# Optimization experiments

Hardware: AMD Instinct MI355X
Metric: run time of the kernel (lower is better)

Reference implementation:

```python
import jax, jax.numpy as jnp
import numpy as np

NUM_TOKENS = 4096
IN_FEATURES = 4096
OUT_FEATURES = 4096
MAX_PACKED = 4


def setup_inputs() -> dict:
    key = jax.random.key(0)
    k1, k2, k3 = jax.random.split(key, 3)
    x = jax.random.normal(k1, (NUM_TOKENS, IN_FEATURES), dtype=jnp.float32)
    weight_stacked = jax.random.normal(
        k2, (MAX_PACKED, OUT_FEATURES, IN_FEATURES), dtype=jnp.float32) * 0.02
    indices = jax.random.randint(k3, (NUM_TOKENS,), 0, MAX_PACKED, dtype=jnp.int32)
    return {"x": x, "weight_stacked": weight_stacked, "indices": indices}


def reference(x, weight_stacked, indices):
    # apply_swap: outputs[t] = x[t] @ weight_stacked[indices[t]].T
    # Grouped-GEMM expressed as E dense GEMMs with masked combine
    # (E = max_packed is a small static constant).
    E = weight_stacked.shape[0]
    out = jnp.zeros((x.shape[0], weight_stacked.shape[1]), dtype=x.dtype)
    for e in range(E):
        sel = (indices == e)[:, None].astype(x.dtype)  # [T,1]
        out = out + sel * jnp.einsum('ti,oi->to', x, weight_stacked[e])
    return out
```

## Files before the change

### kernel.cpp

```cpp
#include <hip/hip_runtime.h>

#define T 4096
#define K 4096
#define O 4096
#define E 4
#define BK 64
#define MAXT128 35

typedef __attribute__((ext_vector_type(8))) short bf16x8;
typedef __attribute__((ext_vector_type(4))) float f32x4;

__device__ __forceinline__ unsigned short f2bf(float f) {
  unsigned int u = __float_as_uint(f);
  u += 0x7fffu + ((u >> 16) & 1u);
  return (unsigned short)(u >> 16);
}

__global__ void build_meta(const int* __restrict__ idx, int* __restrict__ perm,
                           int* __restrict__ meta, int4* __restrict__ t256,
                           int4* __restrict__ t128, int4* __restrict__ sched) {
  const int wave = threadIdx.x >> 6;
  const int lane = threadIdx.x & 63;
  __shared__ int s_off[E + 1];
  __shared__ int rtE[20], rtP[20], rtC[20];
  __shared__ int r_sh;
  int total = 0;
  for (int t0 = 0; t0 < T; t0 += 64)
    total += __popcll(__ballot(idx[t0 + lane] == wave));
  if (lane == 0) s_off[wave + 1] = total;
  __syncthreads();
  if (threadIdx.x == 0) {
    s_off[0] = 0;
    for (int e = 0; e < E; e++) s_off[e + 1] += s_off[e];
  }
  __syncthreads();
  int base = s_off[wave];
  const unsigned long long below = (1ull << lane) - 1ull;
  for (int t0 = 0; t0 < T; t0 += 64) {
    int e = idx[t0 + lane];
    unsigned long long m = __ballot(e == wave);
    if (e == wave) perm[base + __popcll(m & below)] = t0 + lane;
    base += __popcll(m);
  }
  if (threadIdx.x == 0) {
    int n = 0;
    for (int e = 0; e < E; e++) {
      int s = s_off[e], c = s_off[e + 1] - s;
      for (int ro = 0; ro < c; ro += 256) {
        rtE[n] = e; rtP[n] = s + ro; rtC[n] = (c - ro) < 256 ? (c - ro) : 256; n++;
      }
    }
    r_sh = n;
    meta[0] = n * 16;
    int n1 = 0;
    for (int e = 0; e < E; e++) {
      int s = s_off[e], c = s_off[e + 1] - s;
      for (int ro = 0; ro < c; ro += 128)
        t128[n1++] = make_int4(e, s + ro, (c - ro) < 128 ? (c - ro) : 128, 0);
    }
    for (; n1 < MAXT128; n1++) t128[n1] = make_int4(-1, 0, 0, 0);
  }
  __syncthreads();
  const int r = r_sh;
  for (int i = threadIdx.x; i < 16 * r; i += 256)
    t256[i] = make_int4(rtE[i >> 4], rtP[i >> 4], rtC[i >> 4], (i & 15) * 256);
  {
    const int b = threadIdx.x;
    const int ru = r - 16;
    const int xcd = b & 7, s = b >> 3;
    const int rt_ = 4 * (xcd >> 1) + (s >> 3);
    const int nt_ = 8 * (xcd & 1) + (s & 7);
    sched[b * 3 + 0] = make_int4(rt_ * 16 + nt_, 0, 16, 0);
    int sgi = 1, u0 = b * ru, u1 = u0 + ru;
    while (u0 < u1) {
      int tI = 256 + (u0 >> 4), q0 = u0 & 15;
      int avail = 16 - q0, want = u1 - u0;
      int take = want < avail ? want : avail;
      sched[b * 3 + sgi] = make_int4(tI, q0, take, 0);
      sgi++; u0 += take;
    }
    for (; sgi < 3; sgi++) sched[b * 3 + sgi] = make_int4(-1, 0, 0, 0);
  }
}

__global__ void zero_rem(const int* __restrict__ meta, const int4* __restrict__ t256,
                         const int* __restrict__ perm, float* __restrict__ out) {
  const int ntiles = meta[0];
  const int tI = 256 + (int)blockIdx.x / 16;
  if (tI >= ntiles) return;
  const int4 td = t256[tI];
  const int rt = (blockIdx.x & 15) * 16 + ((int)threadIdx.x >> 4);
  if (rt >= td.z) return;
  float4* p = (float4*)(out + (size_t)perm[td.y + rt] * O + td.w) + (threadIdx.x & 15) * 4;
  const float4 z = {0.f, 0.f, 0.f, 0.f};
  p[0] = z; p[1] = z; p[2] = z; p[3] = z;
}

__global__ void convert_kernel(const float4* __restrict__ w4, const float* __restrict__ x,
                               const int* __restrict__ perm,
                               ushort4* __restrict__ wb4, ushort4* __restrict__ xg4) {
  const size_t NW4 = (size_t)E * O * K / 4;
  const size_t NX4 = (size_t)T * K / 4;
  const size_t stride = (size_t)gridDim.x * blockDim.x;
  const size_t t0 = (size_t)blockIdx.x * blockDim.x + threadIdx.x;
  for (size_t i = t0; i < NW4; i += stride) {
    float4 v = w4[i];
    wb4[i] = make_ushort4(f2bf(v.x), f2bf(v.y), f2bf(v.z), f2bf(v.w));
  }
  for (size_t j = t0; j < NX4; j += stride) {
    int p = (int)(j >> 10);
    int c = (int)(j & 1023);
    float4 v = *((const float4*)(x + (size_t)perm[p] * K) + c);
    xg4[j] = make_ushort4(f2bf(v.x), f2bf(v.y), f2bf(v.z), f2bf(v.w));
  }
}

__global__ __launch_bounds__(512, 2)
void gemm8p(const unsigned short* __restrict__ xg, const unsigned short* __restrict__ wbb,
            const int* __restrict__ perm, const int4* __restrict__ t256,
            const int4* __restrict__ sched, float* __restrict__ out) {
  __shared__ unsigned short lds[65536];
  const int bid = blockIdx.x;
  const int tid = threadIdx.x;
  const int wid = tid >> 6, lane = tid & 63;
  const int wr = wid >> 2, wc = wid & 3;
  const int kc4 = lane >> 4;
  unsigned short* ldsw = &lds[wid * 512];

#define GLL(gp, lp) __builtin_amdgcn_global_load_lds( \
    (const __attribute__((address_space(1))) void*)(gp), \
    (__attribute__((address_space(3))) void*)(lp), 16, 0, 0)
#define STAGE_A(bo, kh, ko) do { \
    GLL(srcA0 + (ko) + (kh) * 32, ldsw + (bo) + (kh) * 8192); \
    GLL(srcA1 + (ko) + (kh) * 32, ldsw + (bo) + (kh) * 8192 + 4096); \
  } while (0)
#define STAGE_B(bo, kh, ko) do { \
    GLL(srcB0 + (ko) + (kh) * 32, ldsw + (bo) + 16384 + (kh) * 8192); \
    GLL(srcB1 + (ko) + (kh) * 32, ldsw + (bo) + 16384 + (kh) * 8192 + 4096); \
  } while (0)
#define LOADA(dst, bo, ks, mh) do { _Pragma("unroll") \
    for (int mi = 0; mi < 4; ++mi) \
      dst[mi] = *(const bf16x8*)&lds[(bo) + (ks) * 8192 + aoff[mh][mi]]; } while (0)
#define LOADB(dst, bo, ks) do { _Pragma("unroll") \
    for (int ni = 0; ni < 4; ++ni) \
      dst[ni] = *(const bf16x8*)&lds[(bo) + 16384 + (ks) * 8192 + boff[ni]]; } while (0)
#define MFMA16(A, B, mh) do { _Pragma("unroll") \
    for (int mi = 0; mi < 4; ++mi) _Pragma("unroll") \
      for (int ni = 0; ni < 4; ++ni) \
        acc[(mh) * 4 + mi][ni] = __builtin_amdgcn_mfma_f32_16x16x32_bf16( \
            A[mi], B[ni], acc[(mh) * 4 + mi][ni], 0, 0, 0); } while (0)
#define BAR() do { __builtin_amdgcn_s_barrier(); asm volatile("" ::: "memory"); } while (0)
#define VM4() asm volatile("s_waitcnt vmcnt(4)" ::: "memory")
#define VM0() asm volatile("s_waitcnt vmcnt(0)" ::: "memory")
#define PRIO1() __builtin_amdgcn_s_setprio(1)
#define PRIO0() __builtin_amdgcn_s_setprio(0)

#define KTILE(C, X, koe) do { \
    const int ko = (koe); \
    LOADA(afP, C, 0, 0); LOADB(bfP, C, 0); \
    STAGE_A(X, 0, ko); \
    PRIO1(); MFMA16(afP, bfP, 0); PRIO0(); \
    LOADA(afQ, C, 0, 1); \
    STAGE_B(X, 0, ko); \
    PRIO1(); MFMA16(afQ, bfP, 1); PRIO0(); \
    VM4(); BAR(); \
    LOADA(afP, C, 1, 0); LOADB(bfQ, C, 1); \
    STAGE_A(X, 1, ko); \
    PRIO1(); MFMA16(afP, bfQ, 0); PRIO0(); \
    LOADA(afQ, C, 1, 1); \
    STAGE_B(X, 1, ko); \
    PRIO1(); MFMA16(afQ, bfQ, 1); PRIO0(); \
    VM4(); BAR(); \
  } while (0)

  int aoff[2][4], boff[4];
#pragma unroll
  for (int mh = 0; mh < 2; ++mh)
#pragma unroll
    for (int mi = 0; mi < 4; ++mi) {
      int r = wr * 128 + mh * 64 + mi * 16 + (lane & 15);
      aoff[mh][mi] = (((r >> 1) << 3) + (((((r & 1) << 2) | kc4)) ^ ((r >> 1) & 7))) * 8;
    }
#pragma unroll
  for (int ni = 0; ni < 4; ++ni) {
    int r = wc * 64 + ni * 16 + (lane & 15);
    boff[ni] = (((r >> 1) << 3) + (((((r & 1) << 2) | kc4)) ^ ((r >> 1) & 7))) * 8;
  }

  for (int sg = 0; sg < 3; ++sg) {
    const int4 sd = sched[bid * 3 + sg];
    if (sd.x < 0) break;
    const int4 td = t256[sd.x];
    const int e = td.x, p0 = td.y, rc = td.z, n0 = td.w;
    const int kt0 = sd.y << 2;
    const int nt = sd.z << 2;

    const unsigned short *srcA0, *srcA1, *srcB0, *srcB1;
    {
      const unsigned short* wB = wbb + (size_t)e * O * K + (size_t)n0 * K;
      int s0 = tid, s1 = 512 + tid;
      int b0 = s0 >> 3, v0 = (s0 & 7) ^ (b0 & 7);
      int r0 = b0 * 2 + (v0 >> 2), c0 = v0 & 3;
      int b1 = s1 >> 3, v1 = (s1 & 7) ^ (b1 & 7);
      int r1 = b1 * 2 + (v1 >> 2), c1 = v1 & 3;
      int ra0 = r0 < rc ? r0 : rc - 1;
      int ra1 = r1 < rc ? r1 : rc - 1;
      srcA0 = xg + (size_t)(p0 + ra0) * K + c0 * 8;
      srcA1 = xg + (size_t)(p0 + ra1) * K + c1 * 8;
      srcB0 = wB + (size_t)r0 * K + c0 * 8;
      srcB1 = wB + (size_t)r1 * K + c1 * 8;
    }

    f32x4 acc[8][4] = {};
    bf16x8 afP[4], afQ[4], bfP[4], bfQ[4];

    const int kb = kt0 << 6;
    STAGE_A(0, 0, kb); STAGE_B(0, 0, kb);
    STAGE_A(0, 1, kb); STAGE_B(0, 1, kb);
    VM4(); BAR();

    for (int tp = 0; tp < nt; tp += 2) {
      KTILE(0, 32768, ((tp + 1 < nt ? tp + 1 : tp) + kt0) << 6);
      KTILE(32768, 0, ((tp + 2 < nt ? tp + 2 : tp + 1) + kt0) << 6);
    }
    VM0();

    if (sd.z == 16) {
#pragma unroll
      for (int mh = 0; mh < 2; ++mh)
#pragma unroll
        for (int mi = 0; mi < 4; ++mi) {
          const int rbase = wr * 128 + mh * 64 + mi * 16 + (lane >> 4) * 4;
#pragma unroll
          for (int reg = 0; reg < 4; ++reg) {
            const int pr = rbase + reg;
            if (pr < rc) {
              float* orow = out + (size_t)perm[p0 + pr] * O + n0 + wc * 64 + (lane & 15);
#pragma unroll
              for (int ni = 0; ni < 4; ++ni) orow[ni * 16] = acc[mh * 4 + mi][ni][reg];
            }
          }
        }
    } else {
#pragma unroll
      for (int mh = 0; mh < 2; ++mh)
#pragma unroll
        for (int mi = 0; mi < 4; ++mi) {
          const int rbase = wr * 128 + mh * 64 + mi * 16 + (lane >> 4) * 4;
#pragma unroll
          for (int reg = 0; reg < 4; ++reg) {
            const int pr = rbase + reg;
            if (pr < rc) {
              float* orow = out + (size_t)perm[p0 + pr] * O + n0 + wc * 64 + (lane & 15);
#pragma unroll
              for (int ni = 0; ni < 4; ++ni)
                unsafeAtomicAdd(&orow[ni * 16], acc[mh * 4 + mi][ni][reg]);
            }
          }
        }
    }
  }
}

__global__ __launch_bounds__(256)
void gemm_fb(const float* __restrict__ xf, const float* __restrict__ wf,
             const int* __restrict__ perm, const int4* __restrict__ tiles,
             float* __restrict__ out) {
  __shared__ unsigned short lds_a[128 * 64];
  __shared__ unsigned short lds_b[128 * 64];
  const int4 td = tiles[blockIdx.x];
  if (td.x < 0) return;
  const int e = td.x, p0 = td.y, rc = td.z;
  const int n0 = blockIdx.y * 128;
  const int wave = threadIdx.x >> 6, lane = threadIdx.x & 63;
  const int wr = wave >> 1, wc = wave & 1;
  f32x4 acc[4][4] = {};
  const float* wf_base = wf + (size_t)e * O * K + (size_t)n0 * K;
  for (int k0 = 0; k0 < K; k0 += 64) {
    if (k0) __syncthreads();
#pragma unroll
    for (int i = 0; i < 8; i++) {
      int l4 = i * 256 + (int)threadIdx.x;
      int row = l4 >> 4;
      int c4 = (l4 & 15) << 2;
      int ra = row < rc ? row : (rc - 1);
      const float4 va = *(const float4*)(xf + (size_t)perm[p0 + ra] * K + k0 + c4);
      *(ushort4*)&lds_a[row * 64 + c4] = make_ushort4(f2bf(va.x), f2bf(va.y), f2bf(va.z), f2bf(va.w));
      const float4 vb = *(const float4*)(wf_base + (size_t)row * K + k0 + c4);
      *(ushort4*)&lds_b[row * 64 + c4] = make_ushort4(f2bf(vb.x), f2bf(vb.y), f2bf(vb.z), f2bf(vb.w));
    }
    __syncthreads();
#pragma unroll
    for (int ks = 0; ks < 2; ks++) {
      bf16x8 a2[4], b2[4];
#pragma unroll
      for (int mi = 0; mi < 4; mi++)
        a2[mi] = *(const bf16x8*)&lds_a[(wr * 64 + mi * 16 + (lane & 15)) * 64 + ks * 32 + (lane >> 4) * 8];
#pragma unroll
      for (int ni = 0; ni < 4; ni++)
        b2[ni] = *(const bf16x8*)&lds_b[(wc * 64 + ni * 16 + (lane & 15)) * 64 + ks * 32 + (lane >> 4) * 8];
#pragma unroll
      for (int mi = 0; mi < 4; mi++)
#pragma unroll
        for (int ni = 0; ni < 4; ni++)
          acc[mi][ni] = __builtin_amdgcn_mfma_f32_16x16x32_bf16(a2[mi], b2[ni], acc[mi][ni], 0, 0, 0);
    }
  }
#pragma unroll
  for (int mi = 0; mi < 4; mi++) {
    const int rb = wr * 64 + mi * 16 + (lane >> 4) * 4;
#pragma unroll
    for (int reg = 0; reg < 4; reg++) {
      const int rt = rb + reg;
      if (rt < rc) {
        float* orow = out + (size_t)perm[p0 + rt] * O + n0 + wc * 64 + (lane & 15);
#pragma unroll
        for (int ni = 0; ni < 4; ni++) orow[ni * 16] = acc[mi][ni][reg];
      }
    }
  }
}

extern "C" void kernel_launch(void* const* d_in, const int* in_sizes, int n_in,
                              void* d_out, int out_size, void* d_ws, size_t ws_size,
                              hipStream_t stream) {
  const float* x = (const float*)d_in[0];
  const float* w = (const float*)d_in[1];
  const int* idx = (const int*)d_in[2];
  float* out = (float*)d_out;
  char* ws = (char*)d_ws;

  int* perm = (int*)ws;
  int* meta = (int*)(ws + 16384);
  int4* t256 = (int4*)(ws + 16640);
  int4* t128 = (int4*)(ws + 22528);
  int4* sched = (int4*)(ws + 24576);
  unsigned short* xg = (unsigned short*)(ws + 65536);
  unsigned short* wb = xg + (size_t)T * K;
  const size_t need = 65536 + (size_t)T * K * 2 + (size_t)E * O * K * 2;

  build_meta<<<1, 256, 0, stream>>>(idx, perm, meta, t256, t128, sched);
  if (ws_size >= need) {
    zero_rem<<<768, 256, 0, stream>>>(meta, t256, perm, out);
    convert_kernel<<<4096, 256, 0, stream>>>((const float4*)w, x, perm,
                                             (ushort4*)wb, (ushort4*)xg);
    gemm8p<<<256, 512, 0, stream>>>(xg, wb, perm, t256, sched, out);
  } else {
    gemm_fb<<<dim3(MAXT128, 32), 256, 0, stream>>>(x, w, perm, t128, out);
  }
}
```

Baseline: 269.2 us.

## Shrink GEMM tile to 256x128 with triple-buffered BK=32 pipeline and 512 blocks

Replaces the 256x256 tile GEMM, which used BK=64 double buffering and a 3-segment schedule, with a 256x128 output tile, BK=32 K-steps and a three-stage LDS ring buffer. The grid doubles to 512 blocks at up to 4 blocks per CU. The remainder-tile split-K schedule is rewritten to match, with at most one extra segment per block. This is meant to improve occupancy and load balance and to shorten the per-block critical path. In exchange, each output tile reuses data less, so more global and L2 traffic is needed per FLOP.

```diff
diff --git a/kernel.cpp b/kernel.cpp
--- a/kernel.cpp
+++ b/kernel.cpp
@@ -4,7 +4,6 @@
 #define K 4096
 #define O 4096
 #define E 4
-#define BK 64
 #define MAXT128 35
 
 typedef __attribute__((ext_vector_type(8))) short bf16x8;
@@ -51,7 +50,7 @@
       }
     }
     r_sh = n;
-    meta[0] = n * 16;
+    meta[0] = n * 32;
     int n1 = 0;
     for (int e = 0; e < E; e++) {
       int s = s_off[e], c = s_off[e + 1] - s;
@@ -62,38 +61,34 @@
   }
   __syncthreads();
   const int r = r_sh;
-  for (int i = threadIdx.x; i < 16 * r; i += 256)
-    t256[i] = make_int4(rtE[i >> 4], rtP[i >> 4], rtC[i >> 4], (i & 15) * 256);
-  {
-    const int b = threadIdx.x;
+  for (int i = threadIdx.x; i < 32 * r; i += 256)
+    t256[i] = make_int4(rtE[i >> 5], rtP[i >> 5], rtC[i >> 5], (i & 31) * 128);
+  for (int b = threadIdx.x; b < 512; b += 256) {
     const int ru = r - 16;
     const int xcd = b & 7, s = b >> 3;
-    const int rt_ = 4 * (xcd >> 1) + (s >> 3);
-    const int nt_ = 8 * (xcd & 1) + (s & 7);
-    sched[b * 3 + 0] = make_int4(rt_ * 16 + nt_, 0, 16, 0);
-    int sgi = 1, u0 = b * ru, u1 = u0 + ru;
-    while (u0 < u1) {
-      int tI = 256 + (u0 >> 4), q0 = u0 & 15;
-      int avail = 16 - q0, want = u1 - u0;
-      int take = want < avail ? want : avail;
-      sched[b * 3 + sgi] = make_int4(tI, q0, take, 0);
-      sgi++; u0 += take;
-    }
-    for (; sgi < 3; sgi++) sched[b * 3 + sgi] = make_int4(-1, 0, 0, 0);
+    const int rt_ = 4 * (xcd >> 1) + (s >> 4);
+    const int nt_ = 16 * (xcd & 1) + (s & 15);
+    sched[b * 2 + 0] = make_int4(rt_ * 32 + nt_, 0, 128, 0);
+    const int u0 = (b * ru) >> 2, u1 = ((b + 1) * ru) >> 2;
+    if (u1 > u0) {
+      const int u = u0;
+      sched[b * 2 + 1] = make_int4(512 + (u >> 2), (u & 3) * 32, 32, 0);
+    } else {
+      sched[b * 2 + 1] = make_int4(-1, 0, 0, 0);
+    }
   }
 }
 
 __global__ void zero_rem(const int* __restrict__ meta, const int4* __restrict__ t256,
                          const int* __restrict__ perm, float* __restrict__ out) {
-  const int ntiles = meta[0];
-  const int tI = 256 + (int)blockIdx.x / 16;
-  if (tI >= ntiles) return;
+  const int tI = 512 + (int)blockIdx.x / 16;
+  if (tI >= meta[0]) return;
   const int4 td = t256[tI];
-  const int rt = (blockIdx.x & 15) * 16 + ((int)threadIdx.x >> 4);
-  if (rt >= td.z) return;
-  float4* p = (float4*)(out + (size_t)perm[td.y + rt] * O + td.w) + (threadIdx.x & 15) * 4;
+  const int row = (blockIdx.x & 15) * 16 + ((int)threadIdx.x >> 4);
+  if (row >= td.z) return;
+  float4* p = (float4*)(out + (size_t)perm[td.y + row] * O + td.w) + (threadIdx.x & 15);
   const float4 z = {0.f, 0.f, 0.f, 0.f};
-  p[0] = z; p[1] = z; p[2] = z; p[3] = z;
+  p[0] = z; p[16] = z;
 }
 
 __global__ void convert_kernel(const float4* __restrict__ w4, const float* __restrict__ x,
@@ -115,89 +110,64 @@
   }
 }
 
-__global__ __launch_bounds__(512, 2)
-void gemm8p(const unsigned short* __restrict__ xg, const unsigned short* __restrict__ wbb,
-            const int* __restrict__ perm, const int4* __restrict__ t256,
-            const int4* __restrict__ sched, float* __restrict__ out) {
-  __shared__ unsigned short lds[65536];
+__global__ __launch_bounds__(512, 4)
+void gemm2(const unsigned short* __restrict__ xg, const unsigned short* __restrict__ wbb,
+           const int* __restrict__ perm, const int4* __restrict__ t256,
+           const int4* __restrict__ sched, float* __restrict__ out) {
+  __shared__ unsigned short lds[36864];
   const int bid = blockIdx.x;
   const int tid = threadIdx.x;
   const int wid = tid >> 6, lane = tid & 63;
-  const int wr = wid >> 2, wc = wid & 3;
+  const int wr = wid >> 1, wc = wid & 1;
   const int kc4 = lane >> 4;
-  unsigned short* ldsw = &lds[wid * 512];
 
 #define GLL(gp, lp) __builtin_amdgcn_global_load_lds( \
     (const __attribute__((address_space(1))) void*)(gp), \
     (__attribute__((address_space(3))) void*)(lp), 16, 0, 0)
-#define STAGE_A(bo, kh, ko) do { \
-    GLL(srcA0 + (ko) + (kh) * 32, ldsw + (bo) + (kh) * 8192); \
-    GLL(srcA1 + (ko) + (kh) * 32, ldsw + (bo) + (kh) * 8192 + 4096); \
+#define STAGE(bo, ko) do { \
+    GLL(srcA0 + (ko), &lds[(bo) + wid * 512]); \
+    GLL(srcA1 + (ko), &lds[(bo) + 4096 + wid * 512]); \
+    GLL(srcB0 + (ko), &lds[(bo) + 8192 + wid * 512]); \
   } while (0)
-#define STAGE_B(bo, kh, ko) do { \
-    GLL(srcB0 + (ko) + (kh) * 32, ldsw + (bo) + 16384 + (kh) * 8192); \
-    GLL(srcB1 + (ko) + (kh) * 32, ldsw + (bo) + 16384 + (kh) * 8192 + 4096); \
-  } while (0)
-#define LOADA(dst, bo, ks, mh) do { _Pragma("unroll") \
+#define LOADA(bo) do { _Pragma("unroll") \
     for (int mi = 0; mi < 4; ++mi) \
-      dst[mi] = *(const bf16x8*)&lds[(bo) + (ks) * 8192 + aoff[mh][mi]]; } while (0)
-#define LOADB(dst, bo, ks) do { _Pragma("unroll") \
+      af[mi] = *(const bf16x8*)&lds[(bo) + aoff[mi]]; } while (0)
+#define LOADB(bo) do { _Pragma("unroll") \
     for (int ni = 0; ni < 4; ++ni) \
-      dst[ni] = *(const bf16x8*)&lds[(bo) + 16384 + (ks) * 8192 + boff[ni]]; } while (0)
-#define MFMA16(A, B, mh) do { _Pragma("unroll") \
-    for (int mi = 0; mi < 4; ++mi) _Pragma("unroll") \
-      for (int ni = 0; ni < 4; ++ni) \
-        acc[(mh) * 4 + mi][ni] = __builtin_amdgcn_mfma_f32_16x16x32_bf16( \
-            A[mi], B[ni], acc[(mh) * 4 + mi][ni], 0, 0, 0); } while (0)
+      bf[ni] = *(const bf16x8*)&lds[(bo) + boff[ni]]; } while (0)
+#define MFMA16() do { _Pragma("unroll") \
+    for (int ni = 0; ni < 4; ++ni) _Pragma("unroll") \
+      for (int mi = 0; mi < 4; ++mi) \
+        acc[mi][ni] = __builtin_amdgcn_mfma_f32_16x16x32_bf16( \
+            af[mi], bf[ni], acc[mi][ni], 0, 0, 0); } while (0)
 #define BAR() do { __builtin_amdgcn_s_barrier(); asm volatile("" ::: "memory"); } while (0)
-#define VM4() asm volatile("s_waitcnt vmcnt(4)" ::: "memory")
+#define VM3() asm volatile("s_waitcnt vmcnt(3)" ::: "memory")
 #define VM0() asm volatile("s_waitcnt vmcnt(0)" ::: "memory")
 #define PRIO1() __builtin_amdgcn_s_setprio(1)
 #define PRIO0() __builtin_amdgcn_s_setprio(0)
 
-#define KTILE(C, X, koe) do { \
-    const int ko = (koe); \
-    LOADA(afP, C, 0, 0); LOADB(bfP, C, 0); \
-    STAGE_A(X, 0, ko); \
-    PRIO1(); MFMA16(afP, bfP, 0); PRIO0(); \
-    LOADA(afQ, C, 0, 1); \
-    STAGE_B(X, 0, ko); \
-    PRIO1(); MFMA16(afQ, bfP, 1); PRIO0(); \
-    VM4(); BAR(); \
-    LOADA(afP, C, 1, 0); LOADB(bfQ, C, 1); \
-    STAGE_A(X, 1, ko); \
-    PRIO1(); MFMA16(afP, bfQ, 0); PRIO0(); \
-    LOADA(afQ, C, 1, 1); \
-    STAGE_B(X, 1, ko); \
-    PRIO1(); MFMA16(afQ, bfQ, 1); PRIO0(); \
-    VM4(); BAR(); \
-  } while (0)
-
-  int aoff[2][4], boff[4];
-#pragma unroll
-  for (int mh = 0; mh < 2; ++mh)
-#pragma unroll
-    for (int mi = 0; mi < 4; ++mi) {
-      int r = wr * 128 + mh * 64 + mi * 16 + (lane & 15);
-      aoff[mh][mi] = (((r >> 1) << 3) + (((((r & 1) << 2) | kc4)) ^ ((r >> 1) & 7))) * 8;
-    }
+  int aoff[4], boff[4];
+#pragma unroll
+  for (int mi = 0; mi < 4; ++mi) {
+    int r = wr * 64 + mi * 16 + (lane & 15);
+    aoff[mi] = (((r >> 1) << 3) + (((((r & 1) << 2) | kc4)) ^ ((r >> 1) & 7))) * 8;
+  }
 #pragma unroll
   for (int ni = 0; ni < 4; ++ni) {
     int r = wc * 64 + ni * 16 + (lane & 15);
-    boff[ni] = (((r >> 1) << 3) + (((((r & 1) << 2) | kc4)) ^ ((r >> 1) & 7))) * 8;
-  }
-
-  for (int sg = 0; sg < 3; ++sg) {
-    const int4 sd = sched[bid * 3 + sg];
+    boff[ni] = 8192 + (((r >> 1) << 3) + (((((r & 1) << 2) | kc4)) ^ ((r >> 1) & 7))) * 8;
+  }
+
+  for (int sg = 0; sg < 2; ++sg) {
+    const int4 sd = sched[bid * 2 + sg];
     if (sd.x < 0) break;
     const int4 td = t256[sd.x];
     const int e = td.x, p0 = td.y, rc = td.z, n0 = td.w;
-    const int kt0 = sd.y << 2;
-    const int nt = sd.z << 2;
-
-    const unsigned short *srcA0, *srcA1, *srcB0, *srcB1;
+    const int kt0 = sd.y;
+    const int nt = sd.z;
+
+    const unsigned short *srcA0, *srcA1, *srcB0;
     {
-      const unsigned short* wB = wbb + (size_t)e * O * K + (size_t)n0 * K;
       int s0 = tid, s1 = 512 + tid;
       int b0 = s0 >> 3, v0 = (s0 & 7) ^ (b0 & 7);
       int r0 = b0 * 2 + (v0 >> 2), c0 = v0 & 3;
@@ -207,57 +177,59 @@
       int ra1 = r1 < rc ? r1 : rc - 1;
       srcA0 = xg + (size_t)(p0 + ra0) * K + c0 * 8;
       srcA1 = xg + (size_t)(p0 + ra1) * K + c1 * 8;
+      const unsigned short* wB = wbb + (size_t)e * O * K + (size_t)n0 * K;
       srcB0 = wB + (size_t)r0 * K + c0 * 8;
-      srcB1 = wB + (size_t)r1 * K + c1 * 8;
-    }
-
-    f32x4 acc[8][4] = {};
-    bf16x8 afP[4], afQ[4], bfP[4], bfQ[4];
-
-    const int kb = kt0 << 6;
-    STAGE_A(0, 0, kb); STAGE_B(0, 0, kb);
-    STAGE_A(0, 1, kb); STAGE_B(0, 1, kb);
-    VM4(); BAR();
-
-    for (int tp = 0; tp < nt; tp += 2) {
-      KTILE(0, 32768, ((tp + 1 < nt ? tp + 1 : tp) + kt0) << 6);
-      KTILE(32768, 0, ((tp + 2 < nt ? tp + 2 : tp + 1) + kt0) << 6);
+    }
+
+    f32x4 acc[4][4] = {};
+    bf16x8 af[4], bf[4];
+
+    const int kb = kt0 << 5;
+    STAGE(0, kb);
+    STAGE(12288, kb + 32);
+    VM3(); BAR();
+
+    int bc = 0, bn = 24576;
+    for (int t = 0; t < nt; ++t) {
+      const int tn = (t + 2 < nt ? t + 2 : nt - 1) + kt0;
+      STAGE(bn, tn << 5);
+      LOADA(bc); LOADB(bc);
+      PRIO1(); MFMA16(); PRIO0();
+      VM3(); BAR();
+      bc = (bc == 24576) ? 0 : bc + 12288;
+      bn = (bn == 24576) ? 0 : bn + 12288;
     }
     VM0();
 
-    if (sd.z == 16) {
-#pragma unroll
-      for (int mh = 0; mh < 2; ++mh)
-#pragma unroll
-        for (int mi = 0; mi < 4; ++mi) {
-          const int rbase = wr * 128 + mh * 64 + mi * 16 + (lane >> 4) * 4;
-#pragma unroll
-          for (int reg = 0; reg < 4; ++reg) {
-            const int pr = rbase + reg;
-            if (pr < rc) {
-              float* orow = out + (size_t)perm[p0 + pr] * O + n0 + wc * 64 + (lane & 15);
-#pragma unroll
-              for (int ni = 0; ni < 4; ++ni) orow[ni * 16] = acc[mh * 4 + mi][ni][reg];
-            }
+    if (sd.z == 128) {
+#pragma unroll
+      for (int mi = 0; mi < 4; ++mi) {
+        const int rbase = wr * 64 + mi * 16 + (lane >> 4) * 4;
+#pragma unroll
+        for (int reg = 0; reg < 4; ++reg) {
+          const int pr = rbase + reg;
+          if (pr < rc) {
+            float* orow = out + (size_t)perm[p0 + pr] * O + n0 + wc * 64 + (lane & 15);
+#pragma unroll
+            for (int ni = 0; ni < 4; ++ni) orow[ni * 16] = acc[mi][ni][reg];
           }
         }
+      }
     } else {
 #pragma unroll
-      for (int mh = 0; mh < 2; ++mh)
-#pragma unroll
-        for (int mi = 0; mi < 4; ++mi) {
-          const int rbase = wr * 128 + mh * 64 + mi * 16 + (lane >> 4) * 4;
-#pragma unroll
-          for (int reg = 0; reg < 4; ++reg) {
-            const int pr = rbase + reg;
-            if (pr < rc) {
-              float* orow = out + (size_t)perm[p0 + pr] * O + n0 + wc * 64 + (lane & 15);
-#pragma unroll
-              for (int ni = 0; ni < 4; ++ni)
-                unsafeAtomicAdd(&orow[ni * 16], acc[mh * 4 + mi][ni][reg]);
-            }
+      for (int mi = 0; mi < 4; ++mi) {
+        const int rbase = wr * 64 + mi * 16 + (lane >> 4) * 4;
+#pragma unroll
+        for (int reg = 0; reg < 4; ++reg) {
+          const int pr = rbase + reg;
+          if (pr < rc) {
+            float* orow = out + (size_t)perm[p0 + pr] * O + n0 + wc * 64 + (lane & 15);
+#pragma unroll
+            for (int ni = 0; ni < 4; ++ni)
+              unsafeAtomicAdd(&orow[ni * 16], acc[mi][ni][reg]);
           }
         }
+      }
     }
   }
 }
@@ -333,18 +305,18 @@
   int* perm = (int*)ws;
   int* meta = (int*)(ws + 16384);
   int4* t256 = (int4*)(ws + 16640);
-  int4* t128 = (int4*)(ws + 22528);
-  int4* sched = (int4*)(ws + 24576);
+  int4* t128 = (int4*)(ws + 26624);
+  int4* sched = (int4*)(ws + 28672);
   unsigned short* xg = (unsigned short*)(ws + 65536);
   unsigned short* wb = xg + (size_t)T * K;
   const size_t need = 65536 + (size_t)T * K * 2 + (size_t)E * O * K * 2;
 
   build_meta<<<1, 256, 0, stream>>>(idx, perm, meta, t256, t128, sched);
   if (ws_size >= need) {
-    zero_rem<<<768, 256, 0, stream>>>(meta, t256, perm, out);
+    zero_rem<<<1536, 256, 0, stream>>>(meta, t256, perm, out);
     convert_kernel<<<4096, 256, 0, stream>>>((const float4*)w, x, perm,
                                              (ushort4*)wb, (ushort4*)xg);
-    gemm8p<<<256, 512, 0, stream>>>(xg, wb, perm, t256, sched, out);
+    gemm2<<<512, 512, 0, stream>>>(xg, wb, perm, t256, sched, out);
   } else {
     gemm_fb<<<dim3(MAXT128, 32), 256, 0, stream>>>(x, w, perm, t128, out);
   }
```

Result: slower. 286.3 us (+6.3%).
